# Kernel optimization log

Measured on AMD Instinct MI355X. Metric: run time of the kernel, lower is better.

## Reference

```python
import jax, jax.numpy as jnp
import numpy as np

ALPHA, GAMMA, EPS = 0.25, 2.0, 1e-8
COST_CLASS, COST_BBOX, COST_GIOU = 2.0, 5.0, 2.0


def box_cxcywh_to_xyxy(b):
    cx, cy, w, h = jnp.split(b, 4, axis=-1)
    return jnp.concatenate([cx - 0.5 * w, cy - 0.5 * h, cx + 0.5 * w, cy + 0.5 * h], axis=-1)


def setup_inputs() -> dict:
    key = jax.random.key(0)
    k1, k2, k3, k4 = jax.random.split(key, 4)
    bs, Q, C, T = 16, 900, 80, 1600
    return {
        "pred_logits": jax.random.normal(k1, (bs, Q, C), jnp.float32),
        "pred_boxes": jax.random.uniform(k2, (bs, Q, 4), jnp.float32),
        "tgt_labels": jax.random.randint(k3, (T,), 0, C),
        "tgt_boxes": jax.random.uniform(k4, (T, 4), jnp.float32),
        "g_size": 3,
    }


def reference(pred_logits, pred_boxes, tgt_labels, tgt_boxes, g_size):
    bs, Q, _ = pred_logits.shape
    # focal classification cost (use_focal=True path)
    p = jax.nn.sigmoid(pred_logits.reshape(bs * Q, -1))  # [N, C]
    neg = (1.0 - ALPHA) * p ** GAMMA * (-jnp.log(1.0 - p + EPS))
    pos = ALPHA * (1.0 - p) ** GAMMA * (-jnp.log(p + EPS))
    cost_class = (pos - neg)[:, tgt_labels]  # [N, T]
    # L1 box cost (cdist p=1)
    out_bbox = pred_boxes.reshape(bs * Q, 4)
    cost_bbox = jnp.abs(out_bbox[:, None, :] - tgt_bbox_b(tgt_boxes)).sum(-1)  # [N, T]
    # GIoU cost
    b1 = box_cxcywh_to_xyxy(out_bbox)  # [N, 4]
    b2 = box_cxcywh_to_xyxy(tgt_boxes)  # [T, 4]
    area1 = (b1[:, 2] - b1[:, 0]) * (b1[:, 3] - b1[:, 1])
    area2 = (b2[:, 2] - b2[:, 0]) * (b2[:, 3] - b2[:, 1])
    lt = jnp.maximum(b1[:, None, :2], b2[None, :, :2])
    rb = jnp.minimum(b1[:, None, 2:], b2[None, :, 2:])
    wh = jnp.clip(rb - lt, 0.0)
    inter = wh[..., 0] * wh[..., 1]
    union = area1[:, None] + area2[None, :] - inter
    iou = inter / union
    elt = jnp.minimum(b1[:, None, :2], b2[None, :, :2])
    erb = jnp.maximum(b1[:, None, 2:], b2[None, :, 2:])
    ewh = jnp.clip(erb - elt, 0.0)
    earea = ewh[..., 0] * ewh[..., 1]
    giou = iou - (earea - union) / earea
    # weighted total cost, then group reduction (note: original names it Cmin but takes max over the group dim)
    Cmat = COST_BBOX * cost_bbox + COST_CLASS * cost_class + COST_GIOU * (-giou)
    Cmin = Cmat.reshape(bs, Q // g_size, g_size, -1).max(axis=2)  # [bs, Q//g, T]
    return Cmin


def tgt_bbox_b(tgt_boxes):
    return tgt_boxes[None, :, :]
```

## Files before the change

### kernel.cpp

```cpp
#include <hip/hip_runtime.h>

#define ALPHA 0.25f
#define EPS   1e-8f

constexpr int BS = 16;
constexpr int QN = 900;
constexpr int CN = 80;
constexpr int GS = 3;
constexpr int ROWS = GS;
constexpr int CC_STRIDE = 4;
constexpr int NT_THREADS = 320;

template<int NITER>
__global__ __launch_bounds__(NT_THREADS, 4) void fused_cost_kernel(
    const float* __restrict__ pred_logits,
    const float* __restrict__ pred_boxes,
    const int*   __restrict__ tgt_labels,
    const float* __restrict__ tgt_boxes,
    float*       __restrict__ out,
    int T)
{
    __shared__ __align__(16) float s_cc_t[CN * CC_STRIDE];

    const int tid = threadIdx.x;
    const int qg0 = blockIdx.x;
    const int b   = blockIdx.y;
    const int n0  = b * QN + qg0 * GS;

    const float* lg0 = pred_logits + (size_t)n0 * CN;
    if (tid < (ROWS * CN) / 4) {
        const float4 x4 = ((const float4*)lg0)[tid];
        const int base = tid * 4;
        const int r = base / CN;
        const int c = base - r * CN;
        const float xs[4] = { x4.x, x4.y, x4.z, x4.w };
        #pragma unroll
        for (int i = 0; i < 4; ++i) {
            float p = __fdividef(1.0f, 1.0f + __expf(-xs[i]));
            float omp = 1.0f - p;
            float pos = ALPHA * omp * omp * (-__logf(p + EPS));
            float neg = (1.0f - ALPHA) * p * p * (-__logf(omp + EPS));
            s_cc_t[(c + i) * CC_STRIDE + r] = pos - neg;
        }
    }

    float Px0[ROWS], Py0[ROWS], Px1[ROWS], Py1[ROWS];
    float Pcx2[ROWS], Pcy2[ROWS], Pw[ROWS], Ph[ROWS], Pa[ROWS];
    #pragma unroll
    for (int r = 0; r < ROWS; ++r) {
        const float4 pb = ((const float4*)pred_boxes)[n0 + r];
        Pw[r]   = pb.z;               Ph[r]   = pb.w;
        Pa[r]   = pb.z * pb.w;
        Pcx2[r] = pb.x + pb.x;        Pcy2[r] = pb.y + pb.y;
        Px0[r]  = pb.x - 0.5f * pb.z; Py0[r]  = pb.y - 0.5f * pb.w;
        Px1[r]  = pb.x + 0.5f * pb.z; Py1[r]  = pb.y + 0.5f * pb.w;
    }
    __syncthreads();

    const int qgTotal = QN / GS;
    float* const o0 = out + (size_t)(b * qgTotal + qg0) * T;

    const int nIter = (NITER > 0) ? NITER : ((T + NT_THREADS - 1) / NT_THREADS);

    int t = tid;
    int tl = (NITER > 0) ? t : ((t < T) ? t : (T - 1));
    float4 tr  = ((const float4*)tgt_boxes)[tl];
    int    lab = tgt_labels[tl];

    for (int it = 0; it < nIter; ++it) {
        const int tn = t + NT_THREADS;
        const int tc = (tn < T) ? tn : tl;
        const float4 trn  = ((const float4*)tgt_boxes)[tc];
        const int    labn = tgt_labels[tc];

        const float4 ccq = *((const float4*)&s_cc_t[lab * CC_STRIDE]);
        const float ccv[ROWS] = { ccq.x, ccq.y, ccq.z };

        const float tx0 = tr.x - 0.5f * tr.z, ty0 = tr.y - 0.5f * tr.w;
        const float tx1 = tr.x + 0.5f * tr.z, ty1 = tr.y + 0.5f * tr.w;
        const float ta  = tr.z * tr.w;
        const float tcx2 = tr.x + tr.x, tcy2 = tr.y + tr.y;

        const bool doWrite = (NITER > 0) || (t < T);

        float m = -3.402823466e+38f;
        #pragma unroll
        for (int i = 0; i < ROWS; ++i) {
            const float ix0 = fmaxf(Px0[i], tx0);
            const float iy0 = fmaxf(Py0[i], ty0);
            const float ix1 = fminf(Px1[i], tx1);
            const float iy1 = fminf(Py1[i], ty1);
            const float iw  = fmaxf(ix1 - ix0, 0.0f);
            const float ih  = fmaxf(iy1 - iy0, 0.0f);
            const float inter = iw * ih;

            const float ex0 = fminf(Px0[i], tx0);
            const float ey0 = fminf(Py0[i], ty0);
            const float ex1 = fmaxf(Px1[i], tx1);
            const float ey1 = fmaxf(Py1[i], ty1);
            const float earea = (ex1 - ex0) * (ey1 - ey0);

            const float uni = (Pa[i] + ta) - inter;

            const float h1 = fabsf(Pcx2[i] - tcx2) + fabsf(Pcy2[i] - tcy2);
            const float h2 = fabsf(Pw[i] - tr.z) + fabsf(Ph[i] - tr.w);
            const float l1 = fmaf(0.5f, h1, h2);

            const float num = fmaf(inter, earea, uni * uni);
            const float den = uni * earea;
            const float q   = num * __builtin_amdgcn_rcpf(den);

            const float cost = fmaf(5.0f, l1,
                                fmaf(2.0f, ccv[i], fmaf(-2.0f, q, 2.0f)));
            m = fmaxf(m, cost);
        }
        if (doWrite)
            __builtin_nontemporal_store(m, o0 + t);

        t = tn; tl = tc; tr = trn; lab = labn;
    }
}

extern "C" void kernel_launch(void* const* d_in, const int* in_sizes, int n_in,
                              void* d_out, int out_size, void* d_ws, size_t ws_size,
                              hipStream_t stream) {
    const float* pred_logits = (const float*)d_in[0];
    const float* pred_boxes  = (const float*)d_in[1];
    const int*   tgt_labels  = (const int*)d_in[2];
    const float* tgt_boxes   = (const float*)d_in[3];

    const int T = in_sizes[2];
    float* out = (float*)d_out;

    dim3 grid(QN / GS, BS);
    if (T == NT_THREADS * 5) {
        fused_cost_kernel<5><<<grid, NT_THREADS, 0, stream>>>(
            pred_logits, pred_boxes, tgt_labels, tgt_boxes, out, T);
    } else {
        fused_cost_kernel<0><<<grid, NT_THREADS, 0, stream>>>(
            pred_logits, pred_boxes, tgt_labels, tgt_boxes, out, T);
    }
}
```

Baseline: 90.52 us.

## Assign one query group per wavefront to drop block-wide barrier

Each 64-lane wavefront now owns its own query group, with a private shared-memory class-cost table. This removes the __syncthreads between the logit preprocessing and the main target loop. Each wave now loops 25 times over targets instead of 5, and the grid shrinks by a factor of five. The preprocessing uses scalar loads and is replicated per wave, so it costs more instructions and a larger LDS footprint in exchange for no barrier and longer per-wave streams.

```diff
diff --git a/kernel.cpp b/kernel.cpp
--- a/kernel.cpp
+++ b/kernel.cpp
@@ -9,7 +9,8 @@
 constexpr int GS = 3;
 constexpr int ROWS = GS;
 constexpr int CC_STRIDE = 4;
-constexpr int NT_THREADS = 320;
+constexpr int WPB = 5;
+constexpr int NT_THREADS = WPB * 64;
 
 template<int NITER>
 __global__ __launch_bounds__(NT_THREADS, 4) void fused_cost_kernel(
@@ -20,28 +21,26 @@
     float*       __restrict__ out,
     int T)
 {
-    __shared__ __align__(16) float s_cc_t[CN * CC_STRIDE];
+    __shared__ __align__(16) float s_cc[WPB][CN * CC_STRIDE];
 
-    const int tid = threadIdx.x;
-    const int qg0 = blockIdx.x;
-    const int b   = blockIdx.y;
-    const int n0  = b * QN + qg0 * GS;
+    const int tid  = threadIdx.x;
+    const int w    = tid >> 6;
+    const int lane = tid & 63;
+    const int qg   = blockIdx.x * WPB + w;
+    const int b    = blockIdx.y;
+    const int n0   = b * QN + qg * GS;
 
     const float* lg0 = pred_logits + (size_t)n0 * CN;
-    if (tid < (ROWS * CN) / 4) {
-        const float4 x4 = ((const float4*)lg0)[tid];
-        const int base = tid * 4;
-        const int r = base / CN;
-        const int c = base - r * CN;
-        const float xs[4] = { x4.x, x4.y, x4.z, x4.w };
-        #pragma unroll
-        for (int i = 0; i < 4; ++i) {
-            float p = __fdividef(1.0f, 1.0f + __expf(-xs[i]));
-            float omp = 1.0f - p;
-            float pos = ALPHA * omp * omp * (-__logf(p + EPS));
-            float neg = (1.0f - ALPHA) * p * p * (-__logf(omp + EPS));
-            s_cc_t[(c + i) * CC_STRIDE + r] = pos - neg;
-        }
+    float* const sc = s_cc[w];
+    for (int idx = lane; idx < ROWS * CN; idx += 64) {
+        const float x = lg0[idx];
+        const int r = idx / CN;
+        const int c = idx - r * CN;
+        float p = __fdividef(1.0f, 1.0f + __expf(-x));
+        float omp = 1.0f - p;
+        float pos = ALPHA * omp * omp * (-__logf(p + EPS));
+        float neg = (1.0f - ALPHA) * p * p * (-__logf(omp + EPS));
+        sc[c * CC_STRIDE + r] = pos - neg;
     }
 
     float Px0[ROWS], Py0[ROWS], Px1[ROWS], Py1[ROWS];
@@ -55,25 +54,23 @@
         Px0[r]  = pb.x - 0.5f * pb.z; Py0[r]  = pb.y - 0.5f * pb.w;
         Px1[r]  = pb.x + 0.5f * pb.z; Py1[r]  = pb.y + 0.5f * pb.w;
     }
-    __syncthreads();
 
-    const int qgTotal = QN / GS;
-    float* const o0 = out + (size_t)(b * qgTotal + qg0) * T;
+    float* const o0 = out + (size_t)(b * (QN / GS) + qg) * T;
 
-    const int nIter = (NITER > 0) ? NITER : ((T + NT_THREADS - 1) / NT_THREADS);
+    const int nIter = (NITER > 0) ? NITER : ((T + 63) / 64);
 
-    int t = tid;
+    int t = lane;
     int tl = (NITER > 0) ? t : ((t < T) ? t : (T - 1));
     float4 tr  = ((const float4*)tgt_boxes)[tl];
     int    lab = tgt_labels[tl];
 
     for (int it = 0; it < nIter; ++it) {
-        const int tn = t + NT_THREADS;
+        const int tn = t + 64;
         const int tc = (tn < T) ? tn : tl;
         const float4 trn  = ((const float4*)tgt_boxes)[tc];
         const int    labn = tgt_labels[tc];
 
-        const float4 ccq = *((const float4*)&s_cc_t[lab * CC_STRIDE]);
+        const float4 ccq = *((const float4*)&sc[lab * CC_STRIDE]);
         const float ccv[ROWS] = { ccq.x, ccq.y, ccq.z };
 
         const float tx0 = tr.x - 0.5f * tr.z, ty0 = tr.y - 0.5f * tr.w;
@@ -132,9 +129,9 @@
     const int T = in_sizes[2];
     float* out = (float*)d_out;
 
-    dim3 grid(QN / GS, BS);
-    if (T == NT_THREADS * 5) {
-        fused_cost_kernel<5><<<grid, NT_THREADS, 0, stream>>>(
+    dim3 grid((QN / GS) / WPB, BS);
+    if (T == 64 * 25) {
+        fused_cost_kernel<25><<<grid, NT_THREADS, 0, stream>>>(
             pred_logits, pred_boxes, tgt_labels, tgt_boxes, out, T);
     } else {
         fused_cost_kernel<0><<<grid, NT_THREADS, 0, stream>>>(
```

After: 95.08 us. 5.0% more time.
